# Optimization experiments

Hardware: AMD Instinct MI355X
Metric: run time of the kernel (lower is better)

## Reference

```python
import jax, jax.numpy as jnp
import numpy as np

STEP = 16
LEAK = 32
KSIZE = STEP + LEAK          # 48
PAD = 32                     # ceil((48+16)/2)
THETA = 25.6                 # dense(0.05) * synapses(512) * input_channel(1)
FODEP = 48                   # = kernel_size
BIAS = 0.5
OUT_CH = 1


def setup_inputs() -> dict:
    key = jax.random.key(0)
    k1, k2 = jax.random.split(key, 2)
    input_spikes = (jax.random.uniform(k1, (16, 1, 512, 512)) < 0.05).astype(jnp.float32)
    # weight ~ Exponential(rate=1/w_init) with w_init=0.5, clipped to [0,1]
    u = jax.random.uniform(k2, (1024, 512), minval=1e-6, maxval=1.0)
    weight = jnp.clip(-0.5 * jnp.log(u), 0.0, 1.0)
    return {"input_spikes": input_spikes, "weight": weight}


def _winner_takes_all(potentials):
    # potentials: [B, C, N, T] -> iterate over time with sequential depression state
    p = jnp.transpose(potentials, (3, 1, 0, 2))  # [T, C, B, N]
    T, C, B, N = p.shape

    def step(dep, p_t):
        # dep: [C, B, N] depression counters (integer-valued floats)
        wins = []
        for c in range(C):
            pot = p_t[c] * (dep[c] == 0)                      # mask depressed neurons
            widx = jnp.argmax(pot, axis=-1)                   # [B]
            wval = jnp.take_along_axis(pot, widx[:, None], axis=-1)[:, 0]
            spike = (wval > THETA).astype(pot.dtype)          # [B]
            win = jax.nn.one_hot(widx, N, dtype=pot.dtype) * spike[:, None]  # [B, N]
            # torch: scatter_add(-spike*fodep at winner) then += spike*fodep broadcast
            dep = dep.at[c].add(spike[:, None] * FODEP - win * FODEP)
            # torch: depression += winners[t, c] * fodep (all channels)
            dep = dep + win[None] * FODEP
            wins.append(win)
        dep = jnp.clip(dep - 1.0, 0.0, FODEP - 1.0)
        return dep, jnp.stack(wins, 0)                        # [C, B, N]

    dep0 = jnp.zeros((C, B, N), p.dtype)
    _, winners = jax.lax.scan(step, dep0, p)                  # winners: [T, C, B, N]
    return jnp.transpose(winners, (2, 1, 3, 0))               # [B, C, N, T]


def _forward(input_spikes, weight):
    B, Ci, S, T = input_spikes.shape
    x = input_spikes.reshape(B, Ci * S, T)
    # StepFireLeak.get_weight_kernel
    t = jnp.arange(KSIZE, dtype=weight.dtype)                 # [K]
    t_spike = t / STEP                                        # [K]
    t_leak = -(t - weight[..., None] * STEP) / LEAK + weight[..., None]  # [O, I, K]
    kernel = jnp.maximum(0.0, jnp.minimum(t_spike, t_leak))[..., ::-1]   # [O, I, K] flipped
    pot = jax.lax.conv_general_dilated(
        x, kernel, window_strides=(1,), padding=[(PAD, PAD)],
        dimension_numbers=('NCH', 'OIH', 'NCH'))              # [B, O*N, T']
    N = weight.shape[0] // OUT_CH
    pot = pot.reshape(B, OUT_CH, N, -1) + BIAS * THETA        # labels=None branch
    return _winner_takes_all(pot)


def reference(input_spikes, weight):
    return _forward(input_spikes, weight)
```

## Files before the change

### kernel.cpp

```cpp
#include <hip/hip_runtime.h>
#include <stdint.h>


#define NB 16
#define NI 512
#define NT 512
#define NO 1024
#define TOUT 529
#define SCAP 96
#define OTILE 4
#define PLANE 564
#define DUST 561u
#define THETA_F 25.6f
#define BIAS_T 12.8f

__global__ __launch_bounds__(256) void k_spikes(const float* __restrict__ x,
                                                unsigned short* __restrict__ slist,
                                                unsigned int* __restrict__ spkw,
                                                unsigned int* __restrict__ counts,
                                                float* __restrict__ hg) {
    __shared__ unsigned short sls[4][SCAP];
    int wq = threadIdx.x >> 6, lane = threadIdx.x & 63;
    int row = blockIdx.x * 4 + wq;
    int b = row >> 9;
    const float* xr = x + (size_t)row * NT;
    for (int j = lane; j < SCAP; j += 64) sls[wq][j] = 0xFFFFu;
    int base = 0;
    for (int kk = 0; kk < 8; ++kk) {
        int t = kk * 64 + lane;
        bool pred = xr[t] > 0.5f;
        unsigned long long mask = __ballot(pred);
        int pre = __popcll(mask & ((1ull << lane) - 1ull));
        int pos = base + pre;
        if (pred) {
            if (pos < SCAP) sls[wq][pos] = (unsigned short)t;
            unsafeAtomicAdd(&hg[b * NT + t], 1.0f);
        }
        base += __popcll(mask);
    }
    __syncthreads();
    if (lane < SCAP / 2) {
        unsigned v = (unsigned)sls[wq][2 * lane] | ((unsigned)sls[wq][2 * lane + 1] << 16);
        ((unsigned int*)(slist + (size_t)row * SCAP))[lane] = v;
    }
    if (lane < 32)
        spkw[(size_t)row * 32 + lane] = (unsigned)sls[wq][lane] | ((unsigned)sls[wq][lane + 32] << 16);
    if (lane == 0) counts[row] = (unsigned)min(base, SCAP);
}

__global__ __launch_bounds__(256) void k_taps(const float* __restrict__ weight,
                                              float4* __restrict__ tap) {
    int p = blockIdx.x * 256 + threadIdx.x;
    int o = p >> 9, i = p & 511;
    float w = weight[o * NI + i];
    float b15 = 1.5f * w;
    float vA1 = 0.f, vA2 = 0.f, vB1 = 0.f, vB2 = 0.f;
    int posA = 2000, posB = 2000, state = 0;
    float Km1 = 0.f, Km2 = 0.f;
    for (int tau = 0; tau <= 49; ++tau) {
        float K = 0.f;
        if (tau <= 47) {
            float f = (float)tau * 0.0625f;
            float g = b15 - (float)tau * 0.03125f;
            K = fmaxf(0.f, fminf(f, g));
        }
        float d = (K - Km1) - (Km1 - Km2);
        if (tau == 1) d -= 0.0625f;
        if (d != 0.f) {
            if (state == 0)      { posA = tau; vA1 = d; state = 1; }
            else if (state == 1) { if (tau == posA + 1) { vA2 = d; state = 2; }
                                   else { posB = tau; vB1 = d; state = 3; } }
            else if (state == 2) { posB = tau; vB1 = d; state = 3; }
            else if (state == 3) { if (tau == posB + 1) { vB2 = d; state = 4; } }
        }
        Km2 = Km1; Km1 = K;
    }
    size_t base = 2 * ((size_t)o * NI + i);
    tap[base]     = make_float4(vA1, vA2, __int_as_float(posA), 0.f);
    tap[base + 1] = make_float4(vB1, vB2, __int_as_float(posB), 0.f);
}

#define PROC(TP, WV, CNT, IDX)                                                        \
    {                                                                                 \
        const int p = __float_as_int((TP).z);                                         \
        {                                                                             \
            unsigned e = min((unsigned)((int)((WV) & 0xFFFFu) + p), DUST);            \
            float2* cell = accw + e;                                                  \
            float2 v = *cell; v.x += (TP).x; v.y += (TP).y; *cell = v;                \
        }                                                                             \
        if ((CNT) > 32u) {                                                            \
            unsigned e = min((unsigned)((int)((WV) >> 16) + p), DUST);                \
            float2* cell = accw + e;                                                  \
            float2 v = *cell; v.x += (TP).x; v.y += (TP).y; *cell = v;                \
        }                                                                             \
        if ((CNT) > 64u) {                                                            \
            const unsigned short* sr = slist + (size_t)(b * NI + (IDX)) * SCAP;       \
            for (int kk = 64 + k; kk < (int)(CNT); kk += 32) {                        \
                unsigned e = min((unsigned)((int)sr[kk] + p), DUST);                  \
                float2* cell = accw + e;                                              \
                float2 v = *cell; v.x += (TP).x; v.y += (TP).y; *cell = v;            \
            }                                                                         \
        }                                                                             \
    }

__global__ __launch_bounds__(256, 4) void k_scatter(const unsigned short* __restrict__ slist,
                                                    const unsigned int* __restrict__ spkw,
                                                    const unsigned int* __restrict__ counts,
                                                    const float4* __restrict__ tap,
                                                    const float* __restrict__ hg,
                                                    float* __restrict__ pot) {
    __shared__ __align__(16) float2 acc[OTILE * 2 * PLANE];
    __shared__ double pub[512];
    const int o0 = blockIdx.x * OTILE;
    const int b  = blockIdx.y;
    const int tid = threadIdx.x;
    const int w = tid >> 6, lane = tid & 63;
    const int k = lane >> 1, ramp = lane & 1;

    for (int idx = tid; idx < OTILE * PLANE; idx += 256)
        ((float4*)acc)[idx] = make_float4(0.f, 0.f, 0.f, 0.f);
    __syncthreads();

    float2* accw = acc + (w * 2 + ramp) * PLANE;
    const unsigned int* wrow = spkw + (size_t)(b * NI) * 32 + k;
    const float4* trow = tap + 2 * (size_t)(o0 + w) * NI + ramp;
    const uint4* crow = (const uint4*)(counts + b * NI);

    float4 ntA = trow[0], ntB = trow[2], ntC = trow[4], ntD = trow[6];
    unsigned nwA = wrow[0], nwB = wrow[32], nwC = wrow[64], nwD = wrow[96];
    uint4 ncc = crow[0];

    const int NIQ = NI / 4;
    for (int iq = 0; iq < NIQ; ++iq) {
        const float4 tA = ntA, tB = ntB, tC = ntC, tD = ntD;
        const unsigned wA = nwA, wB = nwB, wC = nwC, wD = nwD;
        const uint4 cc = ncc;
        if (iq + 1 < NIQ) {
            const float4* tb = trow + (size_t)(iq + 1) * 8;
            ntA = tb[0]; ntB = tb[2]; ntC = tb[4]; ntD = tb[6];
            const unsigned int* wb = wrow + (size_t)(iq + 1) * 128;
            nwA = wb[0]; nwB = wb[32]; nwC = wb[64]; nwD = wb[96];
            ncc = crow[iq + 1];
        }
        const int i0 = iq * 4;
        PROC(tA, wA, cc.x, i0)
        PROC(tB, wB, cc.y, i0 + 1)
        PROC(tC, wC, cc.z, i0 + 2)
        PROC(tD, wD, cc.w, i0 + 3)
    }
    __syncthreads();

    const int q = lane;
    const float2* pr0 = acc + (w * 2) * PLANE;
    const float2* pr1 = pr0 + PLANE;
    const float* hb = hg + b * NT;
    double dsv[9];
    double s1d = 0.0, s2d = 0.0;
#pragma unroll
    for (int r = 0; r < 9; ++r) {
        int e = q * 9 + r;
        double d = 0.0;
        if (e < 561) {
            float2 c0 = pr0[e], c1 = pr1[e];
            d = (double)c0.x + (double)c1.x;
            if (e >= 1) {
                float2 m0 = pr0[e - 1], m1 = pr1[e - 1];
                d += (double)m0.y + (double)m1.y;
                if (e <= 512) d += 0.0625 * (double)hb[e - 1];
            }
        }
        dsv[r] = d; s1d += d; s2d += s1d;
    }
    pub[2 * tid] = s1d; pub[2 * tid + 1] = s2d;
    __syncthreads();
    if (tid < 4) {
        double c1 = 0.0, c2 = 0.0;
        for (int qq = 0; qq < 64; ++qq) {
            int j = (tid << 6) + qq;
            double S1 = pub[2 * j], S2 = pub[2 * j + 1];
            pub[2 * j] = c1; pub[2 * j + 1] = c2;
            c2 += 9.0 * c1 + S2;
            c1 += S1;
        }
    }
    __syncthreads();
    {
        const double C1 = pub[2 * tid], C2 = pub[2 * tid + 1];
        double a1 = 0.0, a2 = 0.0;
        float2* rowW = acc + (w * 2) * PLANE;
#pragma unroll
        for (int r = 0; r < 9; ++r) {
            a1 += dsv[r]; a2 += a1;
            int e = q * 9 + r;
            if (e < 561) rowW[e].x = (float)(C2 + C1 * (double)(r + 1) + a2);
        }
    }
    __syncthreads();
    for (int oo = 0; oo < OTILE; ++oo)
        for (int t = tid; t < TOUT; t += 256)
            pot[((size_t)(b * NO + o0 + oo)) * TOUT + t] = acc[(oo * 2) * PLANE + t + 15].x + BIAS_T;
}

__global__ __launch_bounds__(256) void k_argmax(const float* __restrict__ pot,
                                                float* __restrict__ aval,
                                                unsigned short* __restrict__ aidx) {
    __shared__ float sv[4][64];
    __shared__ int   si[4][64];
    int b = blockIdx.y;
    int t0 = blockIdx.x * 64;
    int lane = threadIdx.x & 63, grp = threadIdx.x >> 6;
    int t = t0 + lane;
    bool valid = t < TOUT;
    float best = -1.f; int bidx = 0;
    if (valid) {
        for (int od = 0; od < 256; ++od) {
            int o = grp * 256 + od;
            float v = pot[((size_t)(b * NO + o)) * TOUT + t];
            if (v > best) { best = v; bidx = o; }
        }
    }
    sv[grp][lane] = best; si[grp][lane] = bidx;
    __syncthreads();
    if (grp == 0 && valid) {
#pragma unroll
        for (int g = 1; g < 4; ++g) {
            float v = sv[g][lane];
            if (v > best) { best = v; bidx = si[g][lane]; }
        }
        aval[t * NB + b] = best;
        aidx[t * NB + b] = (unsigned short)bidx;
    }
}

__global__ __launch_bounds__(256) void k_wta(const float* __restrict__ aval,
                                             const unsigned short* __restrict__ aidx,
                                             float* __restrict__ out) {
    __shared__ float lv[TOUT * NB];
    __shared__ unsigned short li[TOUT * NB];
    for (int idx = threadIdx.x; idx < TOUT * NB; idx += 256) { lv[idx] = aval[idx]; li[idx] = aidx[idx]; }
    __syncthreads();
    int b = threadIdx.x;
    if (b < NB) {
        int r = 0;
        for (int t = 0; t < TOUT; ++t) {
            float v = lv[t * NB + b];
            if (r == 0 && v > THETA_F) {
                int n = (int)li[t * NB + b];
                out[((size_t)(b * NO + n)) * TOUT + t] = 1.0f;
                r = 48;
            }
            r = max(r - 1, 0);
        }
    }
}

extern "C" void kernel_launch(void* const* d_in, const int* in_sizes, int n_in,
                              void* d_out, int out_size, void* d_ws, size_t ws_size,
                              hipStream_t stream) {
    const float* x      = (const float*)d_in[0];
    const float* weight = (const float*)d_in[1];
    float* out = (float*)d_out;
    char* ws = (char*)d_ws;
    unsigned short* slist  = (unsigned short*)(ws);
    unsigned int*   spkw   = (unsigned int*)(ws + 1572864);
    unsigned int*   counts = (unsigned int*)(ws + 2621440);
    float4*         tap    = (float4*)(ws + 2654208);
    float*          hg     = (float*)(ws + 19431424);
    float*          aval   = (float*)(ws + 19464192);
    unsigned short* aidx   = (unsigned short*)(ws + 19498048);

    hipMemsetAsync(hg, 0, NB * NT * sizeof(float), stream);
    k_spikes<<<2048, 256, 0, stream>>>(x, slist, spkw, counts, hg);
    k_taps<<<2048, 256, 0, stream>>>(weight, tap);
    k_scatter<<<dim3(NO / OTILE, NB), 256, 0, stream>>>(slist, spkw, counts, tap, hg, out);
    k_argmax<<<dim3(9, 16), 256, 0, stream>>>(out, aval, aidx);
    hipMemsetAsync(d_out, 0, (size_t)out_size * sizeof(float), stream);
    k_wta<<<1, 256, 0, stream>>>(aval, aidx, out);
}
```

Baseline: 517.5 us.

## Split argmax into two stages, shorten tap search, pre-scale scatter offsets

The argmax over 1024 neurons is split into a partial pass over eight channel chunks plus a small reduction kernel, giving many more blocks to fill the GPU. Tap extraction now evaluates the kernel only near its breakpoints instead of scanning all 50 taus. Spike times and tap positions are pre-multiplied by 8 so the scatter can form LDS byte offsets directly. Out-of-range hits go to per-lane spread dump cells to reduce bank conflicts. This costs an extra launch and intermediate buffers.

```diff
diff --git a/kernel.cpp b/kernel.cpp
--- a/kernel.cpp
+++ b/kernel.cpp
@@ -9,8 +9,7 @@
 #define TOUT 529
 #define SCAP 96
 #define OTILE 4
-#define PLANE 564
-#define DUST 561u
+#define PLANE 570
 #define THETA_F 25.6f
 #define BIAS_T 12.8f
 
@@ -24,7 +23,7 @@
     int row = blockIdx.x * 4 + wq;
     int b = row >> 9;
     const float* xr = x + (size_t)row * NT;
-    for (int j = lane; j < SCAP; j += 64) sls[wq][j] = 0xFFFFu;
+    for (int j = lane; j < SCAP; j += 64) sls[wq][j] = 0x1FFF;
     int base = 0;
     for (int kk = 0; kk < 8; ++kk) {
         int t = kk * 64 + lane;
@@ -44,8 +43,16 @@
         ((unsigned int*)(slist + (size_t)row * SCAP))[lane] = v;
     }
     if (lane < 32)
-        spkw[(size_t)row * 32 + lane] = (unsigned)sls[wq][lane] | ((unsigned)sls[wq][lane + 32] << 16);
+        spkw[(size_t)row * 32 + lane] =
+            ((unsigned)sls[wq][lane] << 3) | ((unsigned)sls[wq][lane + 32] << 19);
     if (lane == 0) counts[row] = (unsigned)min(base, SCAP);
+}
+
+__device__ __forceinline__ float kval(float b15, int tau) {
+    if (tau > 47) return 0.f;
+    float f = (float)tau * 0.0625f;
+    float g = b15 - (float)tau * 0.03125f;
+    return fmaxf(0.f, fminf(f, g));
 }
 
 __global__ __launch_bounds__(256) void k_taps(const float* __restrict__ weight,
@@ -55,49 +62,57 @@
     float w = weight[o * NI + i];
     float b15 = 1.5f * w;
     float vA1 = 0.f, vA2 = 0.f, vB1 = 0.f, vB2 = 0.f;
-    int posA = 2000, posB = 2000, state = 0;
-    float Km1 = 0.f, Km2 = 0.f;
-    for (int tau = 0; tau <= 49; ++tau) {
-        float K = 0.f;
-        if (tau <= 47) {
-            float f = (float)tau * 0.0625f;
-            float g = b15 - (float)tau * 0.03125f;
-            K = fmaxf(0.f, fminf(f, g));
-        }
-        float d = (K - Km1) - (Km1 - Km2);
-        if (tau == 1) d -= 0.0625f;
-        if (d != 0.f) {
-            if (state == 0)      { posA = tau; vA1 = d; state = 1; }
-            else if (state == 1) { if (tau == posA + 1) { vA2 = d; state = 2; }
-                                   else { posB = tau; vB1 = d; state = 3; } }
-            else if (state == 2) { posB = tau; vB1 = d; state = 3; }
-            else if (state == 3) { if (tau == posB + 1) { vB2 = d; state = 4; } }
-        }
-        Km2 = Km1; Km1 = K;
-    }
+    int posA = 2048, posB = 2048, state = 0;
+    int n1 = (int)floorf(16.0f * w);
+    int n2 = (int)floorf(48.0f * w);
+    int lo1 = max(n1, 1);
+    int hi1, lo2, hi2;
+    if (n2 <= n1 + 4) { hi1 = min(n2 + 3, 49); lo2 = 1; hi2 = 0; }
+    else             { hi1 = min(n1 + 3, 49); lo2 = n2; hi2 = min(n2 + 3, 49); }
+
+#define TAPRUN(LO, HI)                                                                \
+    {                                                                                 \
+        float Km1 = kval(b15, (LO) - 1), Km2 = kval(b15, (LO) - 2);                   \
+        for (int tau = (LO); tau <= (HI); ++tau) {                                    \
+            float K = kval(b15, tau);                                                 \
+            float d = (K - Km1) - (Km1 - Km2);                                        \
+            if (tau == 1) d -= 0.0625f;                       \
+            if (d != 0.f) {                                                           \
+                if (state == 0)      { posA = tau; vA1 = d; state = 1; }              \
+                else if (state == 1) { if (tau == posA + 1) { vA2 = d; state = 2; }   \
+                                       else { posB = tau; vB1 = d; state = 3; } }     \
+                else if (state == 2) { posB = tau; vB1 = d; state = 3; }              \
+                else if (state == 3) { if (tau == posB + 1) { vB2 = d; state = 4; } } \
+            }                                                                         \
+            Km2 = Km1; Km1 = K;                                                       \
+        }                                                                             \
+    }
+    TAPRUN(lo1, hi1)
+    if (lo2 <= hi2) TAPRUN(lo2, hi2)
+
     size_t base = 2 * ((size_t)o * NI + i);
-    tap[base]     = make_float4(vA1, vA2, __int_as_float(posA), 0.f);
-    tap[base + 1] = make_float4(vB1, vB2, __int_as_float(posB), 0.f);
+    tap[base]     = make_float4(vA1, vA2, __int_as_float(posA >= 2048 ? 16384 : posA * 8), 0.f);
+    tap[base + 1] = make_float4(vB1, vB2, __int_as_float(posB >= 2048 ? 16384 : posB * 8), 0.f);
 }
 
 #define PROC(TP, WV, CNT, IDX)                                                        \
     {                                                                                 \
-        const int p = __float_as_int((TP).z);                                         \
+        const int p8 = __float_as_int((TP).z);                                        \
         {                                                                             \
-            unsigned e = min((unsigned)((int)((WV) & 0xFFFFu) + p), DUST);            \
-            float2* cell = accw + e;                                                  \
+            int e8 = min((int)((WV) & 0xFFFFu) + p8, dcap8);                          \
+            float2* cell = (float2*)((char*)accw + e8);                               \
             float2 v = *cell; v.x += (TP).x; v.y += (TP).y; *cell = v;                \
         }                                                                             \
         if ((CNT) > 32u) {                                                            \
-            unsigned e = min((unsigned)((int)((WV) >> 16) + p), DUST);                \
-            float2* cell = accw + e;                                                  \
+            int e8 = min((int)((WV) >> 16) + p8, dcap8);                              \
+            float2* cell = (float2*)((char*)accw + e8);                               \
             float2 v = *cell; v.x += (TP).x; v.y += (TP).y; *cell = v;                \
         }                                                                             \
         if ((CNT) > 64u) {                                                            \
             const unsigned short* sr = slist + (size_t)(b * NI + (IDX)) * SCAP;       \
             for (int kk = 64 + k; kk < (int)(CNT); kk += 32) {                        \
-                unsigned e = min((unsigned)((int)sr[kk] + p), DUST);                  \
-                float2* cell = accw + e;                                              \
+                int e8 = min(((int)sr[kk] << 3) + p8, dcap8);                         \
+                float2* cell = (float2*)((char*)accw + e8);                           \
                 float2 v = *cell; v.x += (TP).x; v.y += (TP).y; *cell = v;            \
             }                                                                         \
         }                                                                             \
@@ -116,6 +131,7 @@
     const int tid = threadIdx.x;
     const int w = tid >> 6, lane = tid & 63;
     const int k = lane >> 1, ramp = lane & 1;
+    const int dcap8 = (561 + (k & 7)) * 8;
 
     for (int idx = tid; idx < OTILE * PLANE; idx += 256)
         ((float4*)acc)[idx] = make_float4(0.f, 0.f, 0.f, 0.f);
@@ -201,20 +217,20 @@
             pot[((size_t)(b * NO + o0 + oo)) * TOUT + t] = acc[(oo * 2) * PLANE + t + 15].x + BIAS_T;
 }
 
-__global__ __launch_bounds__(256) void k_argmax(const float* __restrict__ pot,
-                                                float* __restrict__ aval,
-                                                unsigned short* __restrict__ aidx) {
+__global__ __launch_bounds__(256) void k_argmax1(const float* __restrict__ pot,
+                                                 float* __restrict__ pval,
+                                                 unsigned short* __restrict__ pidx) {
     __shared__ float sv[4][64];
     __shared__ int   si[4][64];
-    int b = blockIdx.y;
-    int t0 = blockIdx.x * 64;
+    int b = blockIdx.y, c = blockIdx.z;
     int lane = threadIdx.x & 63, grp = threadIdx.x >> 6;
-    int t = t0 + lane;
+    int t = blockIdx.x * 64 + lane;
     bool valid = t < TOUT;
     float best = -1.f; int bidx = 0;
     if (valid) {
-        for (int od = 0; od < 256; ++od) {
-            int o = grp * 256 + od;
+        int ob = c * 128 + grp * 32;
+        for (int od = 0; od < 32; ++od) {
+            int o = ob + od;
             float v = pot[((size_t)(b * NO + o)) * TOUT + t];
             if (v > best) { best = v; bidx = o; }
         }
@@ -227,9 +243,27 @@
             float v = sv[g][lane];
             if (v > best) { best = v; bidx = si[g][lane]; }
         }
-        aval[t * NB + b] = best;
-        aidx[t * NB + b] = (unsigned short)bidx;
-    }
+        pval[((size_t)(c * NB + b)) * TOUT + t] = best;
+        pidx[((size_t)(c * NB + b)) * TOUT + t] = (unsigned short)bidx;
+    }
+}
+
+__global__ __launch_bounds__(64) void k_argmax2(const float* __restrict__ pval,
+                                                const unsigned short* __restrict__ pidx,
+                                                float* __restrict__ aval,
+                                                unsigned short* __restrict__ aidx) {
+    int b = blockIdx.y;
+    int t = blockIdx.x * 64 + threadIdx.x;
+    if (t >= TOUT) return;
+    float best = -1.f; int bidx = 0;
+#pragma unroll
+    for (int c = 0; c < 8; ++c) {
+        size_t idx = ((size_t)(c * NB + b)) * TOUT + t;
+        float v = pval[idx];
+        if (v > best) { best = v; bidx = pidx[idx]; }
+    }
+    aval[t * NB + b] = best;
+    aidx[t * NB + b] = (unsigned short)bidx;
 }
 
 __global__ __launch_bounds__(256) void k_wta(const float* __restrict__ aval,
@@ -268,12 +302,15 @@
     float*          hg     = (float*)(ws + 19431424);
     float*          aval   = (float*)(ws + 19464192);
     unsigned short* aidx   = (unsigned short*)(ws + 19498048);
+    float*          pval   = (float*)(ws + 19514976);
+    unsigned short* pidx   = (unsigned short*)(ws + 19785824);
 
     hipMemsetAsync(hg, 0, NB * NT * sizeof(float), stream);
     k_spikes<<<2048, 256, 0, stream>>>(x, slist, spkw, counts, hg);
     k_taps<<<2048, 256, 0, stream>>>(weight, tap);
     k_scatter<<<dim3(NO / OTILE, NB), 256, 0, stream>>>(slist, spkw, counts, tap, hg, out);
-    k_argmax<<<dim3(9, 16), 256, 0, stream>>>(out, aval, aidx);
+    k_argmax1<<<dim3(9, NB, 8), 256, 0, stream>>>(out, pval, pidx);
+    k_argmax2<<<dim3(9, NB), 64, 0, stream>>>(pval, pidx, aval, aidx);
     hipMemsetAsync(d_out, 0, (size_t)out_size * sizeof(float), stream);
     k_wta<<<1, 256, 0, stream>>>(aval, aidx, out);
 }
```

New measurement: 490.2 us (median of 2 runs). -5.3%, faster.
